# Kernel tuning notes

Measured on AMD Instinct MI355X. Metric: run time of the kernel, lower is better.

## Reference

```python
import jax, jax.numpy as jnp
import numpy as np

D = 1024
H = 16
HD = D // H
EPS = 1e-5


def layer_norm(x, g, b):
    mu = jnp.mean(x, axis=-1, keepdims=True)
    var = jnp.mean((x - mu) ** 2, axis=-1, keepdims=True)
    return (x - mu) * jax.lax.rsqrt(var + EPS) * g + b


def setup_inputs() -> dict:
    key = jax.random.key(0)
    ks = jax.random.split(key, 10)
    s = lambda fan_in: 1.0 / np.sqrt(fan_in)
    inp = {
        "x": jax.random.normal(ks[0], (2, 2048, D), dtype=jnp.float32),
        "w_qkv": jax.random.uniform(ks[1], (D, 3 * D), minval=-s(D), maxval=s(D)),
        "b_qkv": jnp.zeros((3 * D,), jnp.float32),
        "w_fc": jax.random.uniform(ks[2], (D, D), minval=-s(D), maxval=s(D)),
        "b_fc": jnp.zeros((D,), jnp.float32),
        "ln1_g": jnp.ones((D,), jnp.float32),
        "ln1_b": jnp.zeros((D,), jnp.float32),
        "ln2_g": jnp.ones((D,), jnp.float32),
        "ln2_b": jnp.zeros((D,), jnp.float32),
        "w1": jax.random.uniform(ks[3], (D, 4 * D), minval=-s(D), maxval=s(D)),
        "b1": jnp.zeros((4 * D,), jnp.float32),
        "w2": jax.random.uniform(ks[4], (4 * D, D), minval=-s(4 * D), maxval=s(4 * D)),
        "b2": jnp.zeros((D,), jnp.float32),
    }
    return inp


def reference(x, w_qkv, b_qkv, w_fc, b_fc, ln1_g, ln1_b, ln2_g, ln2_b, w1, b1, w2, b2):
    B, T, C = x.shape
    # --- attention sublayer (pre-norm) ---
    h = layer_norm(x, ln1_g, ln1_b)
    qkv = (h @ w_qkv + b_qkv).reshape(B, T, 3, H, HD)
    q, k, v = qkv[:, :, 0], qkv[:, :, 1], qkv[:, :, 2]  # [B,T,H,HD]
    scores = jnp.einsum("bqhd,bkhd->bhqk", q, k) / np.sqrt(HD).astype(np.float32)
    causal = jnp.tril(jnp.ones((T, T), dtype=bool))
    scores = jnp.where(causal, scores, -jnp.inf)
    weights = jax.nn.softmax(scores, axis=-1)
    out = jnp.einsum("bhqk,bkhd->bqhd", weights, v).reshape(B, T, C)
    x = x + out @ w_fc + b_fc
    # --- MLP sublayer (pre-norm) ---
    h = layer_norm(x, ln2_g, ln2_b)
    h = jax.nn.gelu(h @ w1 + b1, approximate=False) @ w2 + b2
    return x + h
```

## Files before the change

### kernel.cpp

```cpp
#include <hip/hip_runtime.h>
#include <hip/hip_bf16.h>
#include <cstdint>
#include <cstddef>

#define SEQ 2048
#define DM  1024

typedef __attribute__((ext_vector_type(8))) __bf16 bf16x8;
typedef __attribute__((ext_vector_type(4))) float  f32x4;
using bf16 = __hip_bfloat16;

__device__ __forceinline__ void gload_lds16(const bf16* g, bf16* l) {
  __builtin_amdgcn_global_load_lds((const __attribute__((address_space(1))) void*)g,
                                   (__attribute__((address_space(3))) void*)l,
                                   16, 0, 0);
}

__global__ void transpose_to_bf16(const float* __restrict__ in, bf16* __restrict__ out,
                                  int K, int N) {
  __shared__ float tile[32][33];
  const int k0 = blockIdx.y * 32, n0 = blockIdx.x * 32;
  const int tx = threadIdx.x, ty = threadIdx.y;
#pragma unroll
  for (int i = ty; i < 32; i += 8)
    tile[i][tx] = in[(size_t)(k0 + i) * N + n0 + tx];
  __syncthreads();
#pragma unroll
  for (int i = ty; i < 32; i += 8)
    out[(size_t)(n0 + i) * K + k0 + tx] = __float2bfloat16(tile[tx][i]);
}

__global__ void ln_to_bf16(const float* __restrict__ x, const float* __restrict__ g,
                           const float* __restrict__ bt, bf16* __restrict__ out) {
  const int row = blockIdx.x;
  const float4 v = ((const float4*)(x + (size_t)row * DM))[threadIdx.x];
  float s  = v.x + v.y + v.z + v.w;
  float s2 = v.x * v.x + v.y * v.y + v.z * v.z + v.w * v.w;
#pragma unroll
  for (int o = 32; o > 0; o >>= 1) { s += __shfl_down(s, o); s2 += __shfl_down(s2, o); }
  __shared__ float red[8];
  const int wave = threadIdx.x >> 6, lane = threadIdx.x & 63;
  if (lane == 0) { red[wave] = s; red[4 + wave] = s2; }
  __syncthreads();
  s  = red[0] + red[1] + red[2] + red[3];
  s2 = red[4] + red[5] + red[6] + red[7];
  const float mu  = s * (1.f / DM);
  const float var = s2 * (1.f / DM) - mu * mu;
  const float r   = rsqrtf(var + 1e-5f);
  const float4 gv = ((const float4*)g)[threadIdx.x];
  const float4 bv = ((const float4*)bt)[threadIdx.x];
  bf16* o = out + (size_t)row * DM + threadIdx.x * 4;
  o[0] = __float2bfloat16((v.x - mu) * r * gv.x + bv.x);
  o[1] = __float2bfloat16((v.y - mu) * r * gv.y + bv.y);
  o[2] = __float2bfloat16((v.z - mu) * r * gv.z + bv.z);
  o[3] = __float2bfloat16((v.w - mu) * r * gv.w + bv.w);
}

enum { EP_BF16 = 0, EP_GELU = 1, EP_RESID = 2 };

template <int MODE>
__global__ void gemm_bt(const bf16* __restrict__ A, const bf16* __restrict__ Bt,
                        const float* __restrict__ bias, const float* __restrict__ resid,
                        float* __restrict__ Cf, bf16* __restrict__ Cb,
                        int M, int N, int K) {
  __shared__ __attribute__((aligned(16))) bf16 As[128 * 32];
  __shared__ __attribute__((aligned(16))) bf16 Bs[128 * 32];
  const int tid  = threadIdx.x;
  const int wave = tid >> 6, lane = tid & 63;
  const int l16 = lane & 15, lq = lane >> 4;
  const int m0 = blockIdx.x * 128, n0 = blockIdx.y * 128;
  const int wr = (wave >> 1) * 64, wc = (wave & 1) * 64;

  f32x4 acc[4][4];
#pragma unroll
  for (int i = 0; i < 4; i++)
#pragma unroll
    for (int j = 0; j < 4; j++) acc[i][j] = 0;

  const int srow = tid >> 2;
  const int scol = (tid & 3) * 8;
  const bf16* ga = A  + (size_t)(m0 + srow) * K + scol;
  const bf16* gb = Bt + (size_t)(n0 + srow) * K + scol;
  bf16* la = As + (size_t)wave * 512;
  bf16* lb = Bs + (size_t)wave * 512;

  for (int kt = 0; kt < K; kt += 32) {
    gload_lds16(ga + kt, la);
    gload_lds16(ga + (size_t)64 * K + kt, la + 2048);
    gload_lds16(gb + kt, lb);
    gload_lds16(gb + (size_t)64 * K + kt, lb + 2048);
    __syncthreads();
    bf16x8 af[4], bfr[4];
#pragma unroll
    for (int mi = 0; mi < 4; mi++)
      af[mi] = *(const bf16x8*)(As + (wr + mi * 16 + l16) * 32 + lq * 8);
#pragma unroll
    for (int ni = 0; ni < 4; ni++)
      bfr[ni] = *(const bf16x8*)(Bs + (wc + ni * 16 + l16) * 32 + lq * 8);
#pragma unroll
    for (int mi = 0; mi < 4; mi++)
#pragma unroll
      for (int ni = 0; ni < 4; ni++)
        acc[mi][ni] = __builtin_amdgcn_mfma_f32_16x16x32_bf16(af[mi], bfr[ni], acc[mi][ni], 0, 0, 0);
    __syncthreads();
  }

#pragma unroll
  for (int ni = 0; ni < 4; ni++) {
    const int col = n0 + wc + ni * 16 + l16;
    const float bb = bias[col];
#pragma unroll
    for (int mi = 0; mi < 4; mi++) {
#pragma unroll
      for (int r = 0; r < 4; r++) {
        const int row = m0 + wr + mi * 16 + lq * 4 + r;
        const size_t idx = (size_t)row * N + col;
        float v = acc[mi][ni][r] + bb;
        if (MODE == EP_BF16) {
          Cb[idx] = __float2bfloat16(v);
        } else if (MODE == EP_GELU) {
          v = 0.5f * v * (1.0f + erff(v * 0.70710678118654752f));
          Cb[idx] = __float2bfloat16(v);
        } else {
          Cf[idx] = resid[idx] + v;
        }
      }
    }
  }
}

#define SCALE_LOG2 0.18033688011112042f

__global__ void flash_attn(const bf16* __restrict__ qkv, bf16* __restrict__ out) {
  const int id = blockIdx.x;
  const int a  = id & 7;
  const int h  = (id >> 3) & 15;
  const int b  = (id >> 7) & 1;
  const int m  = (id >> 8) & 3;
  const int qb = a ^ (((m & 1) * 15) | ((m & 2) << 3));

  const int tid = threadIdx.x;
  const int w = tid >> 6, lane = tid & 63;
  const int l16 = lane & 15, lq = lane >> 4;

  const size_t base = (size_t)b * SEQ * 3072;
  const bf16* Qg = qkv + base + (size_t)h * 64;
  const bf16* Kg = qkv + base + 1024 + (size_t)h * 64;
  const ushort* Vg = (const ushort*)(qkv + base + 2048 + (size_t)h * 64);

  __shared__ __attribute__((aligned(16))) bf16 Qs[64][72];
  __shared__ __attribute__((aligned(16))) bf16 Ks[64][72];
  __shared__ __attribute__((aligned(16))) bf16 VTs[64 * 64];
  __shared__ __attribute__((aligned(16))) bf16 Ps[4][16][72];

  const int q0 = qb * 64;
  const int nkb = qb + 1;

  const int krow = tid >> 2, kcol = (tid & 3) * 16;
  const int vd = tid & 63, vc = tid >> 6;
  const int vsw0 = ((vc ^ (vd & 7)) * 8);
  const int vsw1 = (((vc + 4) ^ (vd & 7)) * 8);

  {
    const int r = tid >> 2, c = (tid & 3) * 16;
    const bf16* src = Qg + (size_t)(q0 + r) * 3072 + c;
    *(uint4*)(&Qs[r][c])     = *(const uint4*)(src);
    *(uint4*)(&Qs[r][c + 8]) = *(const uint4*)(src + 8);

    const bf16* ks = Kg + (size_t)krow * 3072 + kcol;
    const uint4 k0 = *(const uint4*)(ks);
    const uint4 k1 = *(const uint4*)(ks + 8);
    ushort va[8], vb[8];
#pragma unroll
    for (int j = 0; j < 8; j++) va[j] = Vg[(size_t)(vc * 8 + j) * 3072 + vd];
#pragma unroll
    for (int j = 0; j < 8; j++) vb[j] = Vg[(size_t)((vc + 4) * 8 + j) * 3072 + vd];
    *(uint4*)(&Ks[krow][kcol])     = k0;
    *(uint4*)(&Ks[krow][kcol + 8]) = k1;
    uint4 wa, wb;
    wa.x = (uint)va[0] | ((uint)va[1] << 16); wa.y = (uint)va[2] | ((uint)va[3] << 16);
    wa.z = (uint)va[4] | ((uint)va[5] << 16); wa.w = (uint)va[6] | ((uint)va[7] << 16);
    wb.x = (uint)vb[0] | ((uint)vb[1] << 16); wb.y = (uint)vb[2] | ((uint)vb[3] << 16);
    wb.z = (uint)vb[4] | ((uint)vb[5] << 16); wb.w = (uint)vb[6] | ((uint)vb[7] << 16);
    *(uint4*)(&VTs[vd * 64 + vsw0]) = wa;
    *(uint4*)(&VTs[vd * 64 + vsw1]) = wb;
  }
  __syncthreads();

  const bf16x8 qf0 = *(const bf16x8*)(&Qs[w * 16 + l16][lq * 8]);
  const bf16x8 qf1 = *(const bf16x8*)(&Qs[w * 16 + l16][32 + lq * 8]);

  f32x4 oacc[4];
#pragma unroll
  for (int i = 0; i < 4; i++) oacc[i] = 0;
  float lsum[4] = {0.f, 0.f, 0.f, 0.f};

  uint4 kr0, kr1;
  ushort va[8], vb[8];
  const int sw0 = (lq ^ (l16 & 7)) * 8;
  const int sw1 = ((4 + lq) ^ (l16 & 7)) * 8;

  for (int kb = 0; kb < nkb; ++kb) {
    const bool more = (kb + 1 < nkb);

    if (more) {
      const size_t koff = (size_t)((kb + 1) * 64);
      const bf16* ks = Kg + (koff + krow) * 3072 + kcol;
      kr0 = *(const uint4*)(ks);
      kr1 = *(const uint4*)(ks + 8);
#pragma unroll
      for (int j = 0; j < 8; j++) va[j] = Vg[(koff + vc * 8 + j) * 3072 + vd];
#pragma unroll
      for (int j = 0; j < 8; j++) vb[j] = Vg[(koff + (vc + 4) * 8 + j) * 3072 + vd];
    }

    f32x4 sacc[4];
#pragma unroll
    for (int nt = 0; nt < 4; nt++) sacc[nt] = 0;
#pragma unroll
    for (int nt = 0; nt < 4; nt++) {
      const bf16x8 kf0 = *(const bf16x8*)(&Ks[nt * 16 + l16][lq * 8]);
      const bf16x8 kf1 = *(const bf16x8*)(&Ks[nt * 16 + l16][32 + lq * 8]);
      sacc[nt] = __builtin_amdgcn_mfma_f32_16x16x32_bf16(qf0, kf0, sacc[nt], 0, 0, 0);
      sacc[nt] = __builtin_amdgcn_mfma_f32_16x16x32_bf16(qf1, kf1, sacc[nt], 0, 0, 0);
    }

    const bool diag = (kb == qb);
#pragma unroll
    for (int r = 0; r < 4; r++) {
      float e[4];
#pragma unroll
      for (int nt = 0; nt < 4; nt++) {
        float sv = sacc[nt][r] * SCALE_LOG2;
        sv = fminf(sv, 88.f);
        if (diag && (nt * 16 + l16 > w * 16 + lq * 4 + r)) sv = -1e30f;
        e[nt] = exp2f(sv);
        Ps[w][lq * 4 + r][nt * 16 + l16] = __float2bfloat16(e[nt]);
      }
      lsum[r] += (e[0] + e[1]) + (e[2] + e[3]);
    }

    const bf16x8 pf0 = *(const bf16x8*)(&Ps[w][l16][lq * 8]);
    const bf16x8 pf1 = *(const bf16x8*)(&Ps[w][l16][32 + lq * 8]);
#pragma unroll
    for (int dt = 0; dt < 4; dt++) {
      const int d = dt * 16 + l16;
      const bf16x8 vf0 = *(const bf16x8*)(&VTs[d * 64 + sw0]);
      const bf16x8 vf1 = *(const bf16x8*)(&VTs[d * 64 + sw1]);
      oacc[dt] = __builtin_amdgcn_mfma_f32_16x16x32_bf16(pf0, vf0, oacc[dt], 0, 0, 0);
      oacc[dt] = __builtin_amdgcn_mfma_f32_16x16x32_bf16(pf1, vf1, oacc[dt], 0, 0, 0);
    }

    if (more) {
      __syncthreads();
      *(uint4*)(&Ks[krow][kcol])     = kr0;
      *(uint4*)(&Ks[krow][kcol + 8]) = kr1;
      uint4 wa, wb;
      wa.x = (uint)va[0] | ((uint)va[1] << 16); wa.y = (uint)va[2] | ((uint)va[3] << 16);
      wa.z = (uint)va[4] | ((uint)va[5] << 16); wa.w = (uint)va[6] | ((uint)va[7] << 16);
      wb.x = (uint)vb[0] | ((uint)vb[1] << 16); wb.y = (uint)vb[2] | ((uint)vb[3] << 16);
      wb.z = (uint)vb[4] | ((uint)vb[5] << 16); wb.w = (uint)vb[6] | ((uint)vb[7] << 16);
      *(uint4*)(&VTs[vd * 64 + vsw0]) = wa;
      *(uint4*)(&VTs[vd * 64 + vsw1]) = wb;
      __syncthreads();
    }
  }

#pragma unroll
  for (int r = 0; r < 4; r++) {
    float l = lsum[r];
    l += __shfl_xor(l, 1);
    l += __shfl_xor(l, 2);
    l += __shfl_xor(l, 4);
    l += __shfl_xor(l, 8);
    lsum[r] = 1.f / l;
  }
#pragma unroll
  for (int dt = 0; dt < 4; dt++)
#pragma unroll
    for (int r = 0; r < 4; r++) {
      const int qrow = q0 + w * 16 + lq * 4 + r;
      const float v = oacc[dt][r] * lsum[r];
      out[(size_t)(b * SEQ + qrow) * DM + h * 64 + dt * 16 + l16] = __float2bfloat16(v);
    }
}

extern "C" void kernel_launch(void* const* d_in, const int* in_sizes, int n_in,
                              void* d_out, int out_size, void* d_ws, size_t ws_size,
                              hipStream_t stream) {
  const float* x     = (const float*)d_in[0];
  const float* w_qkv = (const float*)d_in[1];
  const float* b_qkv = (const float*)d_in[2];
  const float* w_fc  = (const float*)d_in[3];
  const float* b_fc  = (const float*)d_in[4];
  const float* ln1_g = (const float*)d_in[5];
  const float* ln1_b = (const float*)d_in[6];
  const float* ln2_g = (const float*)d_in[7];
  const float* ln2_b = (const float*)d_in[8];
  const float* w1    = (const float*)d_in[9];
  const float* b1    = (const float*)d_in[10];
  const float* w2    = (const float*)d_in[11];
  const float* b2    = (const float*)d_in[12];
  float* out = (float*)d_out;

  char* ws    = (char*)d_ws;
  float* x2   = (float*)(ws);
  bf16* big   = (bf16*)(ws + (size_t)(16 << 20));
  bf16* small = (bf16*)(ws + (size_t)(48 << 20));
  bf16* wT    = (bf16*)(ws + (size_t)(56 << 20));

  const dim3 tb(32, 8);

  ln_to_bf16<<<dim3(4096), dim3(256), 0, stream>>>(x, ln1_g, ln1_b, small);
  transpose_to_bf16<<<dim3(96, 32), tb, 0, stream>>>(w_qkv, wT, 1024, 3072);
  gemm_bt<EP_BF16><<<dim3(32, 24), dim3(256), 0, stream>>>(
      small, wT, b_qkv, nullptr, nullptr, big, 4096, 3072, 1024);
  flash_attn<<<dim3(1024), dim3(256), 0, stream>>>(big, small);
  transpose_to_bf16<<<dim3(32, 32), tb, 0, stream>>>(w_fc, wT, 1024, 1024);
  gemm_bt<EP_RESID><<<dim3(32, 8), dim3(256), 0, stream>>>(
      small, wT, b_fc, x, x2, nullptr, 4096, 1024, 1024);
  ln_to_bf16<<<dim3(4096), dim3(256), 0, stream>>>(x2, ln2_g, ln2_b, small);
  transpose_to_bf16<<<dim3(128, 32), tb, 0, stream>>>(w1, wT, 1024, 4096);
  gemm_bt<EP_GELU><<<dim3(32, 32), dim3(256), 0, stream>>>(
      small, wT, b1, nullptr, nullptr, big, 4096, 4096, 1024);
  transpose_to_bf16<<<dim3(32, 128), tb, 0, stream>>>(w2, wT, 4096, 1024);
  gemm_bt<EP_RESID><<<dim3(32, 8), dim3(256), 0, stream>>>(
      big, wT, b2, x2, out, nullptr, 4096, 1024, 4096);
}
```

Before: 412.1 us.

## Double-buffer GEMM LDS tiles and use 64-wide N tiles for N=1024 GEMMs

The GEMM kernel now double-buffers its A and B tiles in LDS. It issues the global-to-LDS loads for the next k-step before computing on the current one, and drops one of the two barriers per iteration. The N tile width becomes a template parameter. The two N=1024 GEMMs use 64-wide tiles, which doubles their grid from 256 to 512 blocks for better CU occupancy on the MI355X. The costs are twice the LDS per block, less reuse in the narrower tiles, and reliance on a single barrier being enough to order the async LDS loads against the reads.

```diff
diff --git a/kernel.cpp b/kernel.cpp
--- a/kernel.cpp
+++ b/kernel.cpp
@@ -58,55 +58,71 @@
 
 enum { EP_BF16 = 0, EP_GELU = 1, EP_RESID = 2 };
 
-template <int MODE>
+template <int MODE, int TN>
 __global__ void gemm_bt(const bf16* __restrict__ A, const bf16* __restrict__ Bt,
                         const float* __restrict__ bias, const float* __restrict__ resid,
                         float* __restrict__ Cf, bf16* __restrict__ Cb,
                         int M, int N, int K) {
-  __shared__ __attribute__((aligned(16))) bf16 As[128 * 32];
-  __shared__ __attribute__((aligned(16))) bf16 Bs[128 * 32];
+  constexpr int ABUF = 128 * 32;
+  constexpr int BBUF = TN * 32;
+  constexpr int NI = TN / 32;
+  __shared__ __attribute__((aligned(16))) bf16 As[2 * ABUF];
+  __shared__ __attribute__((aligned(16))) bf16 Bs[2 * BBUF];
   const int tid  = threadIdx.x;
   const int wave = tid >> 6, lane = tid & 63;
   const int l16 = lane & 15, lq = lane >> 4;
-  const int m0 = blockIdx.x * 128, n0 = blockIdx.y * 128;
-  const int wr = (wave >> 1) * 64, wc = (wave & 1) * 64;
-
-  f32x4 acc[4][4];
+  const int m0 = blockIdx.x * 128, n0 = blockIdx.y * TN;
+  const int wr = (wave >> 1) * 64, wc = (wave & 1) * (TN / 2);
+
+  f32x4 acc[4][NI];
 #pragma unroll
   for (int i = 0; i < 4; i++)
 #pragma unroll
-    for (int j = 0; j < 4; j++) acc[i][j] = 0;
+    for (int j = 0; j < NI; j++) acc[i][j] = 0;
 
   const int srow = tid >> 2;
   const int scol = (tid & 3) * 8;
   const bf16* ga = A  + (size_t)(m0 + srow) * K + scol;
   const bf16* gb = Bt + (size_t)(n0 + srow) * K + scol;
-  bf16* la = As + (size_t)wave * 512;
-  bf16* lb = Bs + (size_t)wave * 512;
-
-  for (int kt = 0; kt < K; kt += 32) {
-    gload_lds16(ga + kt, la);
-    gload_lds16(ga + (size_t)64 * K + kt, la + 2048);
-    gload_lds16(gb + kt, lb);
-    gload_lds16(gb + (size_t)64 * K + kt, lb + 2048);
+
+  {
+    bf16* la = As + wave * 512;
+    bf16* lb = Bs + wave * 512;
+    gload_lds16(ga, la);
+    gload_lds16(ga + (size_t)64 * K, la + 2048);
+    gload_lds16(gb, lb);
+    if (TN == 128) gload_lds16(gb + (size_t)64 * K, lb + 2048);
+  }
+
+  const int NKT = K >> 5;
+  for (int it = 0; it < NKT; ++it) {
     __syncthreads();
-    bf16x8 af[4], bfr[4];
+    const int cur = it & 1, nxt = cur ^ 1;
+    if (it + 1 < NKT) {
+      const int kt = (it + 1) << 5;
+      bf16* la = As + nxt * ABUF + wave * 512;
+      bf16* lb = Bs + nxt * BBUF + wave * 512;
+      gload_lds16(ga + kt, la);
+      gload_lds16(ga + (size_t)64 * K + kt, la + 2048);
+      gload_lds16(gb + kt, lb);
+      if (TN == 128) gload_lds16(gb + (size_t)64 * K + kt, lb + 2048);
+    }
+    bf16x8 af[4], bfr[NI];
 #pragma unroll
     for (int mi = 0; mi < 4; mi++)
-      af[mi] = *(const bf16x8*)(As + (wr + mi * 16 + l16) * 32 + lq * 8);
-#pragma unroll
-    for (int ni = 0; ni < 4; ni++)
-      bfr[ni] = *(const bf16x8*)(Bs + (wc + ni * 16 + l16) * 32 + lq * 8);
+      af[mi] = *(const bf16x8*)(As + cur * ABUF + (wr + mi * 16 + l16) * 32 + lq * 8);
+#pragma unroll
+    for (int ni = 0; ni < NI; ni++)
+      bfr[ni] = *(const bf16x8*)(Bs + cur * BBUF + (wc + ni * 16 + l16) * 32 + lq * 8);
 #pragma unroll
     for (int mi = 0; mi < 4; mi++)
 #pragma unroll
-      for (int ni = 0; ni < 4; ni++)
+      for (int ni = 0; ni < NI; ni++)
         acc[mi][ni] = __builtin_amdgcn_mfma_f32_16x16x32_bf16(af[mi], bfr[ni], acc[mi][ni], 0, 0, 0);
-    __syncthreads();
-  }
-
-#pragma unroll
-  for (int ni = 0; ni < 4; ni++) {
+  }
+
+#pragma unroll
+  for (int ni = 0; ni < NI; ni++) {
     const int col = n0 + wc + ni * 16 + l16;
     const float bb = bias[col];
 #pragma unroll
@@ -313,17 +329,17 @@
 
   ln_to_bf16<<<dim3(4096), dim3(256), 0, stream>>>(x, ln1_g, ln1_b, small);
   transpose_to_bf16<<<dim3(96, 32), tb, 0, stream>>>(w_qkv, wT, 1024, 3072);
-  gemm_bt<EP_BF16><<<dim3(32, 24), dim3(256), 0, stream>>>(
+  gemm_bt<EP_BF16, 128><<<dim3(32, 24), dim3(256), 0, stream>>>(
       small, wT, b_qkv, nullptr, nullptr, big, 4096, 3072, 1024);
   flash_attn<<<dim3(1024), dim3(256), 0, stream>>>(big, small);
   transpose_to_bf16<<<dim3(32, 32), tb, 0, stream>>>(w_fc, wT, 1024, 1024);
-  gemm_bt<EP_RESID><<<dim3(32, 8), dim3(256), 0, stream>>>(
+  gemm_bt<EP_RESID, 64><<<dim3(32, 16), dim3(256), 0, stream>>>(
       small, wT, b_fc, x, x2, nullptr, 4096, 1024, 1024);
   ln_to_bf16<<<dim3(4096), dim3(256), 0, stream>>>(x2, ln2_g, ln2_b, small);
   transpose_to_bf16<<<dim3(128, 32), tb, 0, stream>>>(w1, wT, 1024, 4096);
-  gemm_bt<EP_GELU><<<dim3(32, 32), dim3(256), 0, stream>>>(
+  gemm_bt<EP_GELU, 128><<<dim3(32, 32), dim3(256), 0, stream>>>(
       small, wT, b1, nullptr, nullptr, big, 4096, 4096, 1024);
   transpose_to_bf16<<<dim3(32, 128), tb, 0, stream>>>(w2, wT, 4096, 1024);
-  gemm_bt<EP_RESID><<<dim3(32, 8), dim3(256), 0, stream>>>(
+  gemm_bt<EP_RESID, 64><<<dim3(32, 16), dim3(256), 0, stream>>>(
       big, wT, b2, x2, out, nullptr, 4096, 1024, 4096);
 }
```

After: 384.3 us. -6.7%, faster.

## Double-buffer GEMM LDS tiles, swizzle layout, and use 8 waves per block

Applied to the files above, without the earlier changes.

The GEMM now uses two LDS buffers so the global-to-LDS load for the next K tile is issued while the current tile feeds the MFMAs, and it needs only one barrier per iteration. LDS columns are XOR-swizzled on both the write and read sides to avoid bank conflicts. The block grows to 512 threads (8 waves), each computing a 32x64 sub-tile, which lowers per-wave accumulator register use. The cost is twice the LDS per block, and launch_bounds(512,1) may limit how many blocks fit on a CU.

```diff
diff --git a/kernel.cpp b/kernel.cpp
--- a/kernel.cpp
+++ b/kernel.cpp
@@ -59,50 +59,72 @@
 enum { EP_BF16 = 0, EP_GELU = 1, EP_RESID = 2 };
 
 template <int MODE>
+__launch_bounds__(512, 1)
 __global__ void gemm_bt(const bf16* __restrict__ A, const bf16* __restrict__ Bt,
                         const float* __restrict__ bias, const float* __restrict__ resid,
                         float* __restrict__ Cf, bf16* __restrict__ Cb,
                         int M, int N, int K) {
-  __shared__ __attribute__((aligned(16))) bf16 As[128 * 32];
-  __shared__ __attribute__((aligned(16))) bf16 Bs[128 * 32];
+  constexpr int BUF = 128 * 32;
+  __shared__ __attribute__((aligned(16))) bf16 As[2 * BUF];
+  __shared__ __attribute__((aligned(16))) bf16 Bs[2 * BUF];
   const int tid  = threadIdx.x;
   const int wave = tid >> 6, lane = tid & 63;
   const int l16 = lane & 15, lq = lane >> 4;
   const int m0 = blockIdx.x * 128, n0 = blockIdx.y * 128;
-  const int wr = (wave >> 1) * 64, wc = (wave & 1) * 64;
-
-  f32x4 acc[4][4];
-#pragma unroll
-  for (int i = 0; i < 4; i++)
+  const int wr = (wave >> 1) * 32, wc = (wave & 1) * 64;
+
+  f32x4 acc[2][4];
+#pragma unroll
+  for (int i = 0; i < 2; i++)
 #pragma unroll
     for (int j = 0; j < 4; j++) acc[i][j] = 0;
 
   const int srow = tid >> 2;
-  const int scol = (tid & 3) * 8;
-  const bf16* ga = A  + (size_t)(m0 + srow) * K + scol;
-  const bf16* gb = Bt + (size_t)(n0 + srow) * K + scol;
-  bf16* la = As + (size_t)wave * 512;
-  bf16* lb = Bs + (size_t)wave * 512;
-
-  for (int kt = 0; kt < K; kt += 32) {
-    gload_lds16(ga + kt, la);
-    gload_lds16(ga + (size_t)64 * K + kt, la + 2048);
-    gload_lds16(gb + kt, lb);
-    gload_lds16(gb + (size_t)64 * K + kt, lb + 2048);
+  const int sc   = tid & 3;
+  const int scs  = sc ^ ((srow >> 1) & 3);
+  const bf16* ga = A  + (size_t)(m0 + srow) * K + scs * 8;
+  const bf16* gb = Bt + (size_t)(n0 + srow) * K + scs * 8;
+
+  {
+    bf16* la = As + wave * 512;
+    bf16* lb = Bs + wave * 512;
+    gload_lds16(ga, la);
+    gload_lds16(gb, lb);
+  }
+
+  int racol[2], rbcol[4];
+#pragma unroll
+  for (int mi = 0; mi < 2; mi++) {
+    const int ra = wr + mi * 16 + l16;
+    racol[mi] = ra * 32 + (lq ^ ((ra >> 1) & 3)) * 8;
+  }
+#pragma unroll
+  for (int ni = 0; ni < 4; ni++) {
+    const int rb = wc + ni * 16 + l16;
+    rbcol[ni] = rb * 32 + (lq ^ ((rb >> 1) & 3)) * 8;
+  }
+
+  const int NKT = K >> 5;
+  for (int it = 0; it < NKT; ++it) {
     __syncthreads();
-    bf16x8 af[4], bfr[4];
-#pragma unroll
-    for (int mi = 0; mi < 4; mi++)
-      af[mi] = *(const bf16x8*)(As + (wr + mi * 16 + l16) * 32 + lq * 8);
+    const int cur = it & 1, nxt = cur ^ 1;
+    if (it + 1 < NKT) {
+      const int kt = (it + 1) << 5;
+      gload_lds16(ga + kt, As + nxt * BUF + wave * 512);
+      gload_lds16(gb + kt, Bs + nxt * BUF + wave * 512);
+    }
+    bf16x8 af[2], bfr[4];
+#pragma unroll
+    for (int mi = 0; mi < 2; mi++)
+      af[mi] = *(const bf16x8*)(As + cur * BUF + racol[mi]);
 #pragma unroll
     for (int ni = 0; ni < 4; ni++)
-      bfr[ni] = *(const bf16x8*)(Bs + (wc + ni * 16 + l16) * 32 + lq * 8);
-#pragma unroll
-    for (int mi = 0; mi < 4; mi++)
+      bfr[ni] = *(const bf16x8*)(Bs + cur * BUF + rbcol[ni]);
+#pragma unroll
+    for (int mi = 0; mi < 2; mi++)
 #pragma unroll
       for (int ni = 0; ni < 4; ni++)
         acc[mi][ni] = __builtin_amdgcn_mfma_f32_16x16x32_bf16(af[mi], bfr[ni], acc[mi][ni], 0, 0, 0);
-    __syncthreads();
   }
 
 #pragma unroll
@@ -110,7 +132,7 @@
     const int col = n0 + wc + ni * 16 + l16;
     const float bb = bias[col];
 #pragma unroll
-    for (int mi = 0; mi < 4; mi++) {
+    for (int mi = 0; mi < 2; mi++) {
 #pragma unroll
       for (int r = 0; r < 4; r++) {
         const int row = m0 + wr + mi * 16 + lq * 4 + r;
@@ -313,17 +335,17 @@
 
   ln_to_bf16<<<dim3(4096), dim3(256), 0, stream>>>(x, ln1_g, ln1_b, small);
   transpose_to_bf16<<<dim3(96, 32), tb, 0, stream>>>(w_qkv, wT, 1024, 3072);
-  gemm_bt<EP_BF16><<<dim3(32, 24), dim3(256), 0, stream>>>(
+  gemm_bt<EP_BF16><<<dim3(32, 24), dim3(512), 0, stream>>>(
       small, wT, b_qkv, nullptr, nullptr, big, 4096, 3072, 1024);
   flash_attn<<<dim3(1024), dim3(256), 0, stream>>>(big, small);
   transpose_to_bf16<<<dim3(32, 32), tb, 0, stream>>>(w_fc, wT, 1024, 1024);
-  gemm_bt<EP_RESID><<<dim3(32, 8), dim3(256), 0, stream>>>(
+  gemm_bt<EP_RESID><<<dim3(32, 8), dim3(512), 0, stream>>>(
       small, wT, b_fc, x, x2, nullptr, 4096, 1024, 1024);
   ln_to_bf16<<<dim3(4096), dim3(256), 0, stream>>>(x2, ln2_g, ln2_b, small);
   transpose_to_bf16<<<dim3(128, 32), tb, 0, stream>>>(w1, wT, 1024, 4096);
-  gemm_bt<EP_GELU><<<dim3(32, 32), dim3(256), 0, stream>>>(
+  gemm_bt<EP_GELU><<<dim3(32, 32), dim3(512), 0, stream>>>(
       small, wT, b1, nullptr, nullptr, big, 4096, 4096, 1024);
   transpose_to_bf16<<<dim3(32, 128), tb, 0, stream>>>(w2, wT, 4096, 1024);
-  gemm_bt<EP_RESID><<<dim3(32, 8), dim3(256), 0, stream>>>(
+  gemm_bt<EP_RESID><<<dim3(32, 8), dim3(512), 0, stream>>>(
       big, wT, b2, x2, out, nullptr, 4096, 1024, 4096);
 }
```

After: 401.7 us. 2.5% less time.

## Double-buffer GEMM LDS tiles, swizzle layout, and split-K residual GEMMs with atomics

Applied to the files above, without the earlier changes.

The GEMM kernel now double-buffers its A/B shared-memory tiles, issuing the next k-tile's async global-to-LDS loads before the current tile's MFMAs, and drops one barrier per iteration. It also XOR-swizzles the LDS column layout to reduce bank conflicts. The two N=1024 residual GEMMs, which launch only 256 blocks, now use split-K over gridDim.z (2 and 4) and accumulate with float atomicAdd into a buffer pre-filled with the residual by a device memcpy. This raises parallelism on those GEMMs but adds the memcpy traffic, atomic contention and nondeterministic summation order.

```diff
diff --git a/kernel.cpp b/kernel.cpp
--- a/kernel.cpp
+++ b/kernel.cpp
@@ -56,20 +56,23 @@
   o[3] = __float2bfloat16((v.w - mu) * r * gv.w + bv.w);
 }
 
-enum { EP_BF16 = 0, EP_GELU = 1, EP_RESID = 2 };
+enum { EP_BF16 = 0, EP_GELU = 1, EP_ATOMIC = 2 };
 
 template <int MODE>
 __global__ void gemm_bt(const bf16* __restrict__ A, const bf16* __restrict__ Bt,
-                        const float* __restrict__ bias, const float* __restrict__ resid,
+                        const float* __restrict__ bias,
                         float* __restrict__ Cf, bf16* __restrict__ Cb,
                         int M, int N, int K) {
-  __shared__ __attribute__((aligned(16))) bf16 As[128 * 32];
-  __shared__ __attribute__((aligned(16))) bf16 Bs[128 * 32];
+  constexpr int BUF = 128 * 32;
+  __shared__ __attribute__((aligned(16))) bf16 As[2 * BUF];
+  __shared__ __attribute__((aligned(16))) bf16 Bs[2 * BUF];
   const int tid  = threadIdx.x;
   const int wave = tid >> 6, lane = tid & 63;
   const int l16 = lane & 15, lq = lane >> 4;
   const int m0 = blockIdx.x * 128, n0 = blockIdx.y * 128;
   const int wr = (wave >> 1) * 64, wc = (wave & 1) * 64;
+  const int KS = K / gridDim.z;
+  const int kbase = blockIdx.z * KS;
 
   f32x4 acc[4][4];
 #pragma unroll
@@ -78,37 +81,61 @@
     for (int j = 0; j < 4; j++) acc[i][j] = 0;
 
   const int srow = tid >> 2;
-  const int scol = (tid & 3) * 8;
-  const bf16* ga = A  + (size_t)(m0 + srow) * K + scol;
-  const bf16* gb = Bt + (size_t)(n0 + srow) * K + scol;
-  bf16* la = As + (size_t)wave * 512;
-  bf16* lb = Bs + (size_t)wave * 512;
-
-  for (int kt = 0; kt < K; kt += 32) {
-    gload_lds16(ga + kt, la);
-    gload_lds16(ga + (size_t)64 * K + kt, la + 2048);
-    gload_lds16(gb + kt, lb);
-    gload_lds16(gb + (size_t)64 * K + kt, lb + 2048);
+  const int sc   = tid & 3;
+  const int scs  = sc ^ ((srow >> 1) & 3);
+  const bf16* ga = A  + (size_t)(m0 + srow) * K + kbase + scs * 8;
+  const bf16* gb = Bt + (size_t)(n0 + srow) * K + kbase + scs * 8;
+
+  {
+    bf16* la = As + wave * 512;
+    bf16* lb = Bs + wave * 512;
+    gload_lds16(ga, la);
+    gload_lds16(ga + (size_t)64 * K, la + 2048);
+    gload_lds16(gb, lb);
+    gload_lds16(gb + (size_t)64 * K, lb + 2048);
+  }
+
+  int racol[4], rbcol[4];
+#pragma unroll
+  for (int i = 0; i < 4; i++) {
+    const int ra = wr + i * 16 + l16;
+    racol[i] = ra * 32 + (lq ^ ((ra >> 1) & 3)) * 8;
+    const int rb = wc + i * 16 + l16;
+    rbcol[i] = rb * 32 + (lq ^ ((rb >> 1) & 3)) * 8;
+  }
+
+  const int NKT = KS >> 5;
+  for (int it = 0; it < NKT; ++it) {
     __syncthreads();
+    const int cur = it & 1, nxt = cur ^ 1;
+    if (it + 1 < NKT) {
+      const int kt = (it + 1) << 5;
+      bf16* la = As + nxt * BUF + wave * 512;
+      bf16* lb = Bs + nxt * BUF + wave * 512;
+      gload_lds16(ga + kt, la);
+      gload_lds16(ga + (size_t)64 * K + kt, la + 2048);
+      gload_lds16(gb + kt, lb);
+      gload_lds16(gb + (size_t)64 * K + kt, lb + 2048);
+    }
     bf16x8 af[4], bfr[4];
 #pragma unroll
     for (int mi = 0; mi < 4; mi++)
-      af[mi] = *(const bf16x8*)(As + (wr + mi * 16 + l16) * 32 + lq * 8);
+      af[mi] = *(const bf16x8*)(As + cur * BUF + racol[mi]);
 #pragma unroll
     for (int ni = 0; ni < 4; ni++)
-      bfr[ni] = *(const bf16x8*)(Bs + (wc + ni * 16 + l16) * 32 + lq * 8);
+      bfr[ni] = *(const bf16x8*)(Bs + cur * BUF + rbcol[ni]);
 #pragma unroll
     for (int mi = 0; mi < 4; mi++)
 #pragma unroll
       for (int ni = 0; ni < 4; ni++)
         acc[mi][ni] = __builtin_amdgcn_mfma_f32_16x16x32_bf16(af[mi], bfr[ni], acc[mi][ni], 0, 0, 0);
-    __syncthreads();
-  }
-
+  }
+
+  const bool lead = (blockIdx.z == 0);
 #pragma unroll
   for (int ni = 0; ni < 4; ni++) {
     const int col = n0 + wc + ni * 16 + l16;
-    const float bb = bias[col];
+    const float bb = (MODE != EP_ATOMIC || lead) ? bias[col] : 0.f;
 #pragma unroll
     for (int mi = 0; mi < 4; mi++) {
 #pragma unroll
@@ -122,7 +149,7 @@
           v = 0.5f * v * (1.0f + erff(v * 0.70710678118654752f));
           Cb[idx] = __float2bfloat16(v);
         } else {
-          Cf[idx] = resid[idx] + v;
+          atomicAdd(&Cf[idx], v);
         }
       }
     }
@@ -310,20 +337,23 @@
   bf16* wT    = (bf16*)(ws + (size_t)(56 << 20));
 
   const dim3 tb(32, 8);
+  const size_t RESB = (size_t)SEQ * 2 * DM * sizeof(float);
 
   ln_to_bf16<<<dim3(4096), dim3(256), 0, stream>>>(x, ln1_g, ln1_b, small);
   transpose_to_bf16<<<dim3(96, 32), tb, 0, stream>>>(w_qkv, wT, 1024, 3072);
   gemm_bt<EP_BF16><<<dim3(32, 24), dim3(256), 0, stream>>>(
-      small, wT, b_qkv, nullptr, nullptr, big, 4096, 3072, 1024);
+      small, wT, b_qkv, nullptr, big, 4096, 3072, 1024);
   flash_attn<<<dim3(1024), dim3(256), 0, stream>>>(big, small);
   transpose_to_bf16<<<dim3(32, 32), tb, 0, stream>>>(w_fc, wT, 1024, 1024);
-  gemm_bt<EP_RESID><<<dim3(32, 8), dim3(256), 0, stream>>>(
-      small, wT, b_fc, x, x2, nullptr, 4096, 1024, 1024);
+  hipMemcpyAsync(x2, x, RESB, hipMemcpyDeviceToDevice, stream);
+  gemm_bt<EP_ATOMIC><<<dim3(32, 8, 2), dim3(256), 0, stream>>>(
+      small, wT, b_fc, x2, nullptr, 4096, 1024, 1024);
   ln_to_bf16<<<dim3(4096), dim3(256), 0, stream>>>(x2, ln2_g, ln2_b, small);
   transpose_to_bf16<<<dim3(128, 32), tb, 0, stream>>>(w1, wT, 1024, 4096);
   gemm_bt<EP_GELU><<<dim3(32, 32), dim3(256), 0, stream>>>(
-      small, wT, b1, nullptr, nullptr, big, 4096, 4096, 1024);
+      small, wT, b1, nullptr, big, 4096, 4096, 1024);
   transpose_to_bf16<<<dim3(32, 128), tb, 0, stream>>>(w2, wT, 4096, 1024);
-  gemm_bt<EP_RESID><<<dim3(32, 8), dim3(256), 0, stream>>>(
-      big, wT, b2, x2, out, nullptr, 4096, 1024, 4096);
-}
+  hipMemcpyAsync(out, x2, RESB, hipMemcpyDeviceToDevice, stream);
+  gemm_bt<EP_ATOMIC><<<dim3(32, 8, 4), dim3(256), 0, stream>>>(
+      big, wT, b2, out, nullptr, 4096, 1024, 4096);
+}
```

After: 428.7 us. 1.04x slower.
